# Kernel optimization log

Hardware: AMD Instinct MI355X
Metric: run time of the kernel (lower is better)

Reference implementation:

```python
import jax, jax.numpy as jnp
import numpy as np

EMBED_DIM = 1024
NUM_HEADS = 16
HEAD_DIM = EMBED_DIM // NUM_HEADS
B, N = 8, 1024


def setup_inputs() -> dict:
    key = jax.random.key(0)
    k1, k2, k3, k4, k5, k6 = jax.random.split(key, 6)
    scale = 1.0 / np.sqrt(EMBED_DIM)
    return {
        "x": jax.random.normal(k1, (B, N, EMBED_DIM), dtype=jnp.float32),
        "attn_mask": jax.random.normal(k2, (N, N), dtype=jnp.float32) * 0.1,
        "in_proj_weight": jax.random.normal(k3, (3 * EMBED_DIM, EMBED_DIM), dtype=jnp.float32) * scale,
        "in_proj_bias": jax.random.normal(k4, (3 * EMBED_DIM,), dtype=jnp.float32) * 0.02,
        "out_w": jax.random.normal(k5, (EMBED_DIM, EMBED_DIM), dtype=jnp.float32) * scale,
        "out_b": jax.random.normal(k6, (EMBED_DIM,), dtype=jnp.float32) * 0.02,
    }


def reference(x, attn_mask, in_proj_weight, in_proj_bias, out_w, out_b):
    # x: (B, N, C); fused QKV projection as in forward_direct
    Bn, Nn, C = x.shape
    H, D = NUM_HEADS, HEAD_DIM
    qkv = x @ in_proj_weight.T + in_proj_bias            # (B, N, 3C)
    qkv = qkv.reshape(Bn, Nn, 3, H, D).transpose(2, 0, 3, 1, 4)  # (3, B, H, N, D)
    q, k, v = qkv[0], qkv[1], qkv[2]
    q = q / jnp.sqrt(jnp.asarray(D, dtype=q.dtype))
    attn = jnp.einsum("bhnd,bhmd->bhnm", q, k)           # (B, H, N, N) scores
    attn = attn + attn_mask                              # broadcast over (B, H)
    attn = jax.nn.softmax(attn, axis=-1)
    out = jnp.einsum("bhnm,bhmd->bhnd", attn, v)         # (B, H, N, D)
    out = out.transpose(0, 2, 1, 3).reshape(Bn, Nn, C)   # (B, N, C)
    return out @ out_w.T + out_b
```

## Files before the change

### kernel.cpp

```cpp
#include <hip/hip_runtime.h>


typedef __bf16 bf16x8 __attribute__((ext_vector_type(8)));
typedef float f32x4 __attribute__((ext_vector_type(4)));
typedef float f32x16 __attribute__((ext_vector_type(16)));
typedef unsigned short us4v __attribute__((ext_vector_type(4)));
typedef unsigned int u32x4 __attribute__((ext_vector_type(4)));

#define MFMA16 __builtin_amdgcn_mfma_f32_16x16x32_bf16
#define MFMA32 __builtin_amdgcn_mfma_f32_32x32x16_bf16

__device__ __forceinline__ unsigned short f2bf(float f) {
    return __builtin_bit_cast(unsigned short, (__bf16)f);
}

__device__ __forceinline__ us4v cvt4(float4 v) {
    us4v r;
    r.x = f2bf(v.x); r.y = f2bf(v.y); r.z = f2bf(v.z); r.w = f2bf(v.w);
    return r;
}

__device__ __forceinline__ unsigned cvtpk(float lo, float hi) {
    unsigned r;
    asm volatile("v_cvt_pk_bf16_f32 %0, %1, %2" : "=v"(r) : "v"(lo), "v"(hi));
    return r;
}

__device__ __forceinline__ void gl16(const unsigned short* g, unsigned short* l) {
    __builtin_amdgcn_global_load_lds(
        (const __attribute__((address_space(1))) unsigned*)g,
        (__attribute__((address_space(3))) unsigned*)l, 16, 0, 0);
}

__global__ __launch_bounds__(256)
void cvt_bf16(const float* __restrict__ src, unsigned short* __restrict__ dst,
              int n4) {
    const int i = blockIdx.x * 256 + threadIdx.x;
    if (i < n4) {
        float4 v = ((const float4*)src)[i];
        ((us4v*)dst)[i] = cvt4(v);
    }
}

__global__ __launch_bounds__(256)
void scale_f32(const float* __restrict__ src, float* __restrict__ dst, int n4) {
    const int i = blockIdx.x * 256 + threadIdx.x;
    if (i < n4) {
        float4 v = ((const float4*)src)[i];
        const float s = 1.4426950408889634f;
        v.x *= s; v.y *= s; v.z *= s; v.w *= s;
        ((float4*)dst)[i] = v;
    }
}

__global__ __launch_bounds__(256, 3)
void qkv_gemm(const unsigned short* __restrict__ xb,
              const unsigned short* __restrict__ wb,
              const float* __restrict__ bias,
              unsigned short* __restrict__ qb, unsigned short* __restrict__ kb,
              unsigned short* __restrict__ vbT)
{
    __shared__ unsigned short lsa[3][128 * 32];
    __shared__ unsigned short lsb[3][128 * 32];
    const int tid  = threadIdx.x;
    const int wave = tid >> 6, lane = tid & 63;
    const int quad = lane >> 4, l15 = lane & 15;
    const int rch = (quad ^ ((l15 >> 1) & 3)) * 8;
    const int m0 = blockIdx.x * 128, n0 = blockIdx.y * 128;
    const int wm = (wave & 1) * 64, wn = (wave >> 1) * 64;

    const int srow = wave * 32 + (lane >> 2);
    const int scol = ((lane & 3) ^ ((lane >> 3) & 3)) * 8;
    const unsigned short* ga = xb + (size_t)(m0 + srow) * 1024 + scol;
    const unsigned short* gb = wb + (size_t)(n0 + srow) * 1024 + scol;
    const int so0 = (wave * 32) * 32;
    const int so1 = (wave * 32 + 16) * 32;

    f32x4 acc[4][4];
#pragma unroll
    for (int i = 0; i < 4; ++i)
#pragma unroll
        for (int j = 0; j < 4; ++j) acc[i][j] = (f32x4){0.f, 0.f, 0.f, 0.f};

    gl16(ga, &lsa[0][so0]);
    gl16(ga + 16 * 1024, &lsa[0][so1]);
    gl16(gb, &lsb[0][so0]);
    gl16(gb + 16 * 1024, &lsb[0][so1]);
    gl16(ga + 32, &lsa[1][so0]);
    gl16(ga + 16 * 1024 + 32, &lsa[1][so1]);
    gl16(gb + 32, &lsb[1][so0]);
    gl16(gb + 16 * 1024 + 32, &lsb[1][so1]);

    for (int kt = 0; kt < 32; ++kt) {
        const int cb = kt % 3;
        if (kt < 30) {
            const int k0 = (kt + 2) * 32;
            const int sb = (kt + 2) % 3;
            gl16(ga + k0, &lsa[sb][so0]);
            gl16(ga + 16 * 1024 + k0, &lsa[sb][so1]);
            gl16(gb + k0, &lsb[sb][so0]);
            gl16(gb + 16 * 1024 + k0, &lsb[sb][so1]);
            asm volatile("s_waitcnt vmcnt(8)" ::: "memory");
        } else if (kt == 30) {
            asm volatile("s_waitcnt vmcnt(4)" ::: "memory");
        } else {
            asm volatile("s_waitcnt vmcnt(0)" ::: "memory");
        }
        __builtin_amdgcn_s_barrier();

        const unsigned short* pa = lsa[cb];
        const unsigned short* pb = lsb[cb];
        bf16x8 af[4], bfr[4];
#pragma unroll
        for (int i = 0; i < 4; ++i)
            af[i] = *(const bf16x8*)&pa[(wm + i * 16 + l15) * 32 + rch];
#pragma unroll
        for (int j = 0; j < 4; ++j)
            bfr[j] = *(const bf16x8*)&pb[(wn + j * 16 + l15) * 32 + rch];
#pragma unroll
        for (int i = 0; i < 4; ++i)
#pragma unroll
            for (int j = 0; j < 4; ++j)
                acc[i][j] = MFMA16(af[i], bfr[j], acc[i][j], 0, 0, 0);

        asm volatile("s_waitcnt lgkmcnt(0)" ::: "memory");
        __builtin_amdgcn_sched_barrier(0);
        __builtin_amdgcn_s_barrier();
    }

    const int which = n0 >> 10;
    if (which == 2) {
#pragma unroll
        for (int j = 0; j < 4; ++j) {
            const int n = n0 + wn + j * 16 + l15;
            const int c = n & 1023;
            const int h = c >> 6, d = c & 63;
            const float bv = bias[n];
#pragma unroll
            for (int i = 0; i < 4; ++i) {
                const int m = m0 + wm + i * 16 + quad * 4;
                const int b = m >> 10, s = m & 1023;
                us4v pk;
#pragma unroll
                for (int r = 0; r < 4; ++r) pk[r] = f2bf(acc[i][j][r] + bv);
                *(us4v*)&vbT[(size_t)((b * 16 + h) * 64 + d) * 1024 + s] = pk;
            }
        }
    } else {
        unsigned short* __restrict__ dst = (which == 0) ? qb : kb;
        const float sc = (which == 0) ? 0.18033688011112442f : 1.0f;
#pragma unroll
        for (int j = 0; j < 4; ++j) {
            const int n = n0 + wn + j * 16 + l15;
            const int c = n & 1023;
            const int h = c >> 6, d = c & 63;
            const float bv = bias[n];
#pragma unroll
            for (int i = 0; i < 4; ++i)
#pragma unroll
                for (int r = 0; r < 4; ++r) {
                    const int m = m0 + wm + i * 16 + quad * 4 + r;
                    const int b = m >> 10, s = m & 1023;
                    const float v = (acc[i][j][r] + bv) * sc;
                    dst[(size_t)((b * 16 + h) * 1024 + s) * 64 + d] = f2bf(v);
                }
        }
    }
}

__global__ __launch_bounds__(256, 3)
void attn_kernel(const unsigned short* __restrict__ qb,
                 const unsigned short* __restrict__ kb,
                 const unsigned short* __restrict__ vbT,
                 const float* __restrict__ mask2,
                 unsigned short* __restrict__ ob)
{
    __shared__ unsigned short lsk[2][2][64 * 32];
    __shared__ unsigned short lsv[2][2][64 * 32];
    const int tid  = threadIdx.x;
    const int wave = tid >> 6, lane = tid & 63;
    const int r5 = lane & 31, hl = lane >> 5;
    const int rs = ((r5 >> 1) ^ (r5 >> 3)) & 3;
    const int p  = blockIdx.x;
    const int lg = (p & 7) * 128 + (p >> 3);
    const int bh = lg >> 3;
    const int q0 = (lg & 7) * 128;
    const int b = bh >> 4, head = bh & 15;

    const unsigned short* __restrict__ kbase = kb + (size_t)bh * 65536;
    const unsigned short* __restrict__ vtb  = vbT + (size_t)bh * 65536;

    const int scol =
        ((lane & 3) ^ ((lane >> 3) & 3) ^ ((2 * wave + (lane >> 5)) & 3)) * 8;
    const unsigned short* gk = kbase + (size_t)(wave * 16 + (lane >> 2)) * 64
                                     + scol;
    const unsigned short* gv = vtb + (size_t)(wave * 16 + (lane >> 2)) * 1024
                                   + scol;
    const int so = (wave * 16) * 32;

    const int q = q0 + wave * 32 + r5;
    bf16x8 bq[4];
    {
        const unsigned short* qrow = qb + (size_t)(bh * 1024 + q) * 64;
#pragma unroll
        for (int kk = 0; kk < 4; ++kk)
            bq[kk] = *(const bf16x8*)(qrow + kk * 16 + hl * 8);
    }

    float lsum = 0.f;
    f32x16 acc[2];
#pragma unroll
    for (int dt = 0; dt < 2; ++dt)
#pragma unroll
        for (int r = 0; r < 16; ++r) acc[dt][r] = 0.f;

    const float* __restrict__ mq = mask2 + (size_t)q * 1024;

    gl16(gk, &lsk[0][0][so]);
    gl16(gk + 32, &lsk[0][1][so]);
    gl16(gv, &lsv[0][0][so]);
    gl16(gv + 32, &lsv[0][1][so]);
    __syncthreads();

    int buf = 0;
    for (int kt = 0; kt < 16; ++kt) {
        f32x16 msk[2];
#pragma unroll
        for (int t32 = 0; t32 < 2; ++t32)
#pragma unroll
            for (int oct = 0; oct < 4; ++oct) {
                const float4 mv = *(const float4*)
                    &mq[kt * 64 + t32 * 32 + oct * 8 + hl * 4];
                msk[t32][4 * oct + 0] = mv.x;
                msk[t32][4 * oct + 1] = mv.y;
                msk[t32][4 * oct + 2] = mv.z;
                msk[t32][4 * oct + 3] = mv.w;
            }
        __builtin_amdgcn_sched_barrier(0);
        if (kt < 15) {
            gl16(gk + (size_t)(kt + 1) * 4096, &lsk[buf ^ 1][0][so]);
            gl16(gk + (size_t)(kt + 1) * 4096 + 32, &lsk[buf ^ 1][1][so]);
            gl16(gv + (size_t)(kt + 1) * 64, &lsv[buf ^ 1][0][so]);
            gl16(gv + (size_t)(kt + 1) * 64 + 32, &lsv[buf ^ 1][1][so]);
        }

#pragma unroll
        for (int t32 = 0; t32 < 2; ++t32) {
            f32x16 s = msk[t32];
            __builtin_amdgcn_s_setprio(1);
#pragma unroll
            for (int kk = 0; kk < 4; ++kk) {
                const unsigned short* kp = lsk[buf][kk >> 1];
                const int c4 = 2 * (kk & 1) + hl;
                const bf16x8 ka = *(const bf16x8*)
                    &kp[(t32 * 32 + r5) * 32 + ((c4 ^ rs) * 8)];
                s = MFMA32(ka, bq[kk], s, 0, 0, 0);
            }
            __builtin_amdgcn_s_setprio(0);

            float pv[16];
            float ts = 0.f;
#pragma unroll
            for (int r = 0; r < 16; ++r) {
                pv[r] = exp2f(s[r]);
                ts += pv[r];
            }
            lsum += ts;

            bf16x8 pfr[2];
#pragma unroll
            for (int cl = 0; cl < 2; ++cl) {
                unsigned xa = cvtpk(pv[8 * cl + 0], pv[8 * cl + 1]);
                unsigned xb = cvtpk(pv[8 * cl + 2], pv[8 * cl + 3]);
                unsigned ya = cvtpk(pv[8 * cl + 4], pv[8 * cl + 5]);
                unsigned yb = cvtpk(pv[8 * cl + 6], pv[8 * cl + 7]);
                asm volatile("v_permlane32_swap_b32 %0, %1"
                             : "+v"(xa), "+v"(ya));
                asm volatile("v_permlane32_swap_b32 %0, %1"
                             : "+v"(xb), "+v"(yb));
                const u32x4 t = {xa, xb, ya, yb};
                pfr[cl] = __builtin_bit_cast(bf16x8, t);
            }

            __builtin_amdgcn_s_setprio(1);
#pragma unroll
            for (int cl = 0; cl < 2; ++cl) {
                const int cg = t32 * 2 + cl;
                const unsigned short* vp = lsv[buf][cg >> 1];
                const int c4v = 2 * (cg & 1) + hl;
                const int voff = (c4v ^ rs) * 8;
#pragma unroll
                for (int dt = 0; dt < 2; ++dt) {
                    const bf16x8 va = *(const bf16x8*)
                        &vp[(dt * 32 + r5) * 32 + voff];
                    acc[dt] = MFMA32(va, pfr[cl], acc[dt], 0, 0, 0);
                }
            }
            __builtin_amdgcn_s_setprio(0);
        }

        __syncthreads();
        buf ^= 1;
    }

    lsum += __shfl_xor(lsum, 32, 64);
    const float inv = 1.0f / lsum;

    unsigned short* orow =
        ob + (size_t)(b * 1024 + q) * 1024 + head * 64;
#pragma unroll
    for (int dt = 0; dt < 2; ++dt)
#pragma unroll
        for (int oct = 0; oct < 4; ++oct) {
            us4v o;
#pragma unroll
            for (int r = 0; r < 4; ++r)
                o[r] = f2bf(acc[dt][4 * oct + r] * inv);
            *(us4v*)&orow[dt * 32 + oct * 8 + hl * 4] = o;
        }
}

__global__ __launch_bounds__(256, 3)
void out_gemm(const unsigned short* __restrict__ a,
              const unsigned short* __restrict__ wb,
              const float* __restrict__ bias, float* __restrict__ out)
{
    __shared__ unsigned short lsa[3][128 * 32];
    __shared__ unsigned short lsb[3][128 * 32];
    const int tid  = threadIdx.x;
    const int wave = tid >> 6, lane = tid & 63;
    const int quad = lane >> 4, l15 = lane & 15;
    const int rch = (quad ^ ((l15 >> 1) & 3)) * 8;
    const int m0 = blockIdx.x * 128, n0 = blockIdx.y * 128;
    const int wm = (wave & 1) * 64, wn = (wave >> 1) * 64;

    const int srow = wave * 32 + (lane >> 2);
    const int scol = ((lane & 3) ^ ((lane >> 3) & 3)) * 8;
    const unsigned short* ga = a + (size_t)(m0 + srow) * 1024 + scol;
    const unsigned short* gb = wb + (size_t)(n0 + srow) * 1024 + scol;
    const int so0 = (wave * 32) * 32;
    const int so1 = (wave * 32 + 16) * 32;

    f32x4 acc[4][4];
#pragma unroll
    for (int i = 0; i < 4; ++i)
#pragma unroll
        for (int j = 0; j < 4; ++j) acc[i][j] = (f32x4){0.f, 0.f, 0.f, 0.f};

    gl16(ga, &lsa[0][so0]);
    gl16(ga + 16 * 1024, &lsa[0][so1]);
    gl16(gb, &lsb[0][so0]);
    gl16(gb + 16 * 1024, &lsb[0][so1]);
    gl16(ga + 32, &lsa[1][so0]);
    gl16(ga + 16 * 1024 + 32, &lsa[1][so1]);
    gl16(gb + 32, &lsb[1][so0]);
    gl16(gb + 16 * 1024 + 32, &lsb[1][so1]);

    for (int kt = 0; kt < 32; ++kt) {
        const int cb = kt % 3;
        if (kt < 30) {
            const int k0 = (kt + 2) * 32;
            const int sb = (kt + 2) % 3;
            gl16(ga + k0, &lsa[sb][so0]);
            gl16(ga + 16 * 1024 + k0, &lsa[sb][so1]);
            gl16(gb + k0, &lsb[sb][so0]);
            gl16(gb + 16 * 1024 + k0, &lsb[sb][so1]);
            asm volatile("s_waitcnt vmcnt(8)" ::: "memory");
        } else if (kt == 30) {
            asm volatile("s_waitcnt vmcnt(4)" ::: "memory");
        } else {
            asm volatile("s_waitcnt vmcnt(0)" ::: "memory");
        }
        __builtin_amdgcn_s_barrier();

        const unsigned short* pa = lsa[cb];
        const unsigned short* pb = lsb[cb];
        bf16x8 af[4], bfr[4];
#pragma unroll
        for (int i = 0; i < 4; ++i)
            af[i] = *(const bf16x8*)&pa[(wm + i * 16 + l15) * 32 + rch];
#pragma unroll
        for (int j = 0; j < 4; ++j)
            bfr[j] = *(const bf16x8*)&pb[(wn + j * 16 + l15) * 32 + rch];
#pragma unroll
        for (int i = 0; i < 4; ++i)
#pragma unroll
            for (int j = 0; j < 4; ++j)
                acc[i][j] = MFMA16(af[i], bfr[j], acc[i][j], 0, 0, 0);

        asm volatile("s_waitcnt lgkmcnt(0)" ::: "memory");
        __builtin_amdgcn_sched_barrier(0);
        __builtin_amdgcn_s_barrier();
    }

#pragma unroll
    for (int j = 0; j < 4; ++j) {
        const int n = n0 + wn + j * 16 + l15;
        const float bv = bias[n];
#pragma unroll
        for (int i = 0; i < 4; ++i)
#pragma unroll
            for (int r = 0; r < 4; ++r) {
                const int m = m0 + wm + i * 16 + quad * 4 + r;
                out[(size_t)m * 1024 + n] = acc[i][j][r] + bv;
            }
    }
}

extern "C" void kernel_launch(void* const* d_in, const int* in_sizes, int n_in,
                              void* d_out, int out_size, void* d_ws, size_t ws_size,
                              hipStream_t stream) {
    const float* x    = (const float*)d_in[0];
    const float* mask = (const float*)d_in[1];
    const float* win  = (const float*)d_in[2];
    const float* bin  = (const float*)d_in[3];
    const float* wout = (const float*)d_in[4];
    const float* bout = (const float*)d_in[5];
    float* out = (float*)d_out;

    char* ws = (char*)d_ws;
    unsigned short* xb = (unsigned short*)(ws);
    unsigned short* ob = (unsigned short*)(ws);
    unsigned short* qb = (unsigned short*)(ws + (size_t)(16 << 20));
    unsigned short* kb = (unsigned short*)(ws + (size_t)(32 << 20));
    unsigned short* vbT = (unsigned short*)(ws + (size_t)(48 << 20));
    unsigned short* winb  = (unsigned short*)d_out;
    float* mask2 = (float*)((char*)d_out + (size_t)(6 << 20));
    unsigned short* woutb = qb;

    cvt_bf16<<<dim3(8192), 256, 0, stream>>>(x, xb, 8 * 1024 * 1024 / 4);
    cvt_bf16<<<dim3(3072), 256, 0, stream>>>(win, winb, 3 * 1024 * 1024 / 4);
    scale_f32<<<dim3(1024), 256, 0, stream>>>(mask, mask2, 1024 * 1024 / 4);
    qkv_gemm<<<dim3(64, 24), 256, 0, stream>>>(xb, winb, bin, qb, kb, vbT);
    attn_kernel<<<dim3(1024), 256, 0, stream>>>(qb, kb, vbT, mask2, ob);
    cvt_bf16<<<dim3(1024), 256, 0, stream>>>(wout, woutb, 1024 * 1024 / 4);
    out_gemm<<<dim3(64, 8), 256, 0, stream>>>(ob, woutb, bout, out);
}
```

Measured before the change: 280.2 us.

## Restructure QKV GEMM into 256x128 tiles with 512 threads and interleaved prefetch

The QKV projection GEMM now uses 512-thread blocks covering 256x128 output tiles, with a 64-wide K step split into two 32-wide LDS sub-buffers and double buffering. Global-to-LDS loads for the next K step are spread between the two MFMA phases, MFMA sections run at raised wave priority, and a remapped 1D grid groups blocks per XCD for L2 reuse. The aim is to reuse each weight tile across more rows and hide load latency better. The cost is more LDS per block and lower occupancy, and the epilogue's wm/wn layout changed, which has to stay consistent with the per-wave tile mapping.

```diff
diff --git a/kernel.cpp b/kernel.cpp
--- a/kernel.cpp
+++ b/kernel.cpp
@@ -53,28 +53,36 @@
     }
 }
 
-__global__ __launch_bounds__(256, 3)
+__global__ __launch_bounds__(512, 2)
 void qkv_gemm(const unsigned short* __restrict__ xb,
               const unsigned short* __restrict__ wb,
               const float* __restrict__ bias,
               unsigned short* __restrict__ qb, unsigned short* __restrict__ kb,
               unsigned short* __restrict__ vbT)
 {
-    __shared__ unsigned short lsa[3][128 * 32];
-    __shared__ unsigned short lsb[3][128 * 32];
+    __shared__ unsigned short lA[2][2][256 * 32];
+    __shared__ unsigned short lB[2][2][128 * 32];
     const int tid  = threadIdx.x;
     const int wave = tid >> 6, lane = tid & 63;
     const int quad = lane >> 4, l15 = lane & 15;
     const int rch = (quad ^ ((l15 >> 1) & 3)) * 8;
-    const int m0 = blockIdx.x * 128, n0 = blockIdx.y * 128;
-    const int wm = (wave & 1) * 64, wn = (wave >> 1) * 64;
-
-    const int srow = wave * 32 + (lane >> 2);
-    const int scol = ((lane & 3) ^ ((lane >> 3) & 3)) * 8;
-    const unsigned short* ga = xb + (size_t)(m0 + srow) * 1024 + scol;
-    const unsigned short* gb = wb + (size_t)(n0 + srow) * 1024 + scol;
-    const int so0 = (wave * 32) * 32;
-    const int so1 = (wave * 32 + 16) * 32;
+    const int p  = blockIdx.x;
+    const int lg = (p & 7) * 96 + (p >> 3);
+    const int m0 = (lg & 31) * 256, n0 = (lg >> 5) * 128;
+    const int wm = (wave >> 1) * 64, wn = (wave & 1) * 64;
+
+    const int drow = tid >> 2;
+    const int dch  = (tid & 3) * 8;
+    const int gch  = ((tid & 3) ^ ((tid >> 3) & 3)) * 8;
+
+    const unsigned short* gA = xb + (size_t)(m0 + drow) * 1024 + gch;
+    const unsigned short* gB = wb + (size_t)(n0 + drow) * 1024 + gch;
+
+#define SA(bf, ks, s, kt)                                                     \
+    gl16(gA + (size_t)(s) * 128 * 1024 + (kt) * 64 + (ks) * 32,               \
+         &lA[bf][ks][((s) * 128 + drow) * 32 + dch])
+#define SB(bf, ks, kt)                                                        \
+    gl16(gB + (kt) * 64 + (ks) * 32, &lB[bf][ks][drow * 32 + dch])
 
     f32x4 acc[4][4];
 #pragma unroll
@@ -82,51 +90,48 @@
 #pragma unroll
         for (int j = 0; j < 4; ++j) acc[i][j] = (f32x4){0.f, 0.f, 0.f, 0.f};
 
-    gl16(ga, &lsa[0][so0]);
-    gl16(ga + 16 * 1024, &lsa[0][so1]);
-    gl16(gb, &lsb[0][so0]);
-    gl16(gb + 16 * 1024, &lsb[0][so1]);
-    gl16(ga + 32, &lsa[1][so0]);
-    gl16(ga + 16 * 1024 + 32, &lsa[1][so1]);
-    gl16(gb + 32, &lsb[1][so0]);
-    gl16(gb + 16 * 1024 + 32, &lsb[1][so1]);
-
-    for (int kt = 0; kt < 32; ++kt) {
-        const int cb = kt % 3;
-        if (kt < 30) {
-            const int k0 = (kt + 2) * 32;
-            const int sb = (kt + 2) % 3;
-            gl16(ga + k0, &lsa[sb][so0]);
-            gl16(ga + 16 * 1024 + k0, &lsa[sb][so1]);
-            gl16(gb + k0, &lsb[sb][so0]);
-            gl16(gb + 16 * 1024 + k0, &lsb[sb][so1]);
-            asm volatile("s_waitcnt vmcnt(8)" ::: "memory");
-        } else if (kt == 30) {
-            asm volatile("s_waitcnt vmcnt(4)" ::: "memory");
+    SA(0, 0, 0, 0); SA(0, 0, 1, 0); SB(0, 0, 0);
+    SA(0, 1, 0, 0); SA(0, 1, 1, 0); SB(0, 1, 0);
+
+    int cur = 0;
+    for (int kt = 0; kt < 16; ++kt) {
+        if (kt < 15) {
+            SA(cur ^ 1, 0, 0, kt + 1);
+            SA(cur ^ 1, 0, 1, kt + 1);
+            asm volatile("s_waitcnt vmcnt(2)" ::: "memory");
         } else {
             asm volatile("s_waitcnt vmcnt(0)" ::: "memory");
         }
         __builtin_amdgcn_s_barrier();
 
-        const unsigned short* pa = lsa[cb];
-        const unsigned short* pb = lsb[cb];
-        bf16x8 af[4], bfr[4];
-#pragma unroll
-        for (int i = 0; i < 4; ++i)
-            af[i] = *(const bf16x8*)&pa[(wm + i * 16 + l15) * 32 + rch];
-#pragma unroll
-        for (int j = 0; j < 4; ++j)
-            bfr[j] = *(const bf16x8*)&pb[(wn + j * 16 + l15) * 32 + rch];
-#pragma unroll
-        for (int i = 0; i < 4; ++i)
+#pragma unroll
+        for (int ks = 0; ks < 2; ++ks) {
+            const unsigned short* pA = lA[cur][ks];
+            const unsigned short* pB = lB[cur][ks];
+            bf16x8 af[4], bfr[4];
+#pragma unroll
+            for (int i = 0; i < 4; ++i)
+                af[i] = *(const bf16x8*)&pA[(wm + i * 16 + l15) * 32 + rch];
 #pragma unroll
             for (int j = 0; j < 4; ++j)
-                acc[i][j] = MFMA16(af[i], bfr[j], acc[i][j], 0, 0, 0);
-
-        asm volatile("s_waitcnt lgkmcnt(0)" ::: "memory");
-        __builtin_amdgcn_sched_barrier(0);
-        __builtin_amdgcn_s_barrier();
-    }
+                bfr[j] = *(const bf16x8*)&pB[(wn + j * 16 + l15) * 32 + rch];
+            if (kt < 15) {
+                if (ks == 0) { SB(cur ^ 1, 0, kt + 1); SA(cur ^ 1, 1, 0, kt + 1); }
+                else         { SA(cur ^ 1, 1, 1, kt + 1); SB(cur ^ 1, 1, kt + 1); }
+            }
+            __builtin_amdgcn_s_setprio(1);
+#pragma unroll
+            for (int i = 0; i < 4; ++i)
+#pragma unroll
+                for (int j = 0; j < 4; ++j)
+                    acc[i][j] = MFMA16(af[i], bfr[j], acc[i][j], 0, 0, 0);
+            __builtin_amdgcn_s_setprio(0);
+            __builtin_amdgcn_s_barrier();
+        }
+        cur ^= 1;
+    }
+#undef SA
+#undef SB
 
     const int which = n0 >> 10;
     if (which == 2) {
@@ -431,7 +436,7 @@
     cvt_bf16<<<dim3(8192), 256, 0, stream>>>(x, xb, 8 * 1024 * 1024 / 4);
     cvt_bf16<<<dim3(3072), 256, 0, stream>>>(win, winb, 3 * 1024 * 1024 / 4);
     scale_f32<<<dim3(1024), 256, 0, stream>>>(mask, mask2, 1024 * 1024 / 4);
-    qkv_gemm<<<dim3(64, 24), 256, 0, stream>>>(xb, winb, bin, qb, kb, vbT);
+    qkv_gemm<<<dim3(768), 512, 0, stream>>>(xb, winb, bin, qb, kb, vbT);
     attn_kernel<<<dim3(1024), 256, 0, stream>>>(qb, kb, vbT, mask2, ob);
     cvt_bf16<<<dim3(1024), 256, 0, stream>>>(wout, woutb, 1024 * 1024 / 4);
     out_gemm<<<dim3(64, 8), 256, 0, stream>>>(ob, woutb, bout, out);
```

New measurement: 315.4 us. 12.6% more time.
